# Kernel optimization log

Measured on AMD Instinct MI355X. Metric: run time of the kernel, lower is better.

Reference implementation:

```python
import jax, jax.numpy as jnp
import numpy as np

# Config (matches init_kwargs)
D_MODEL = 1024
D_MLP = 4096
N_EXPERTS = 8
TOP_K = 2  # experts_per_token
BATCH = 1
POS = 2048


def setup_inputs() -> dict:
    key = jax.random.key(0)
    k0, k1, k2, k3, k4 = jax.random.split(key, 5)
    s = 0.02  # typical init scale
    x = jax.random.normal(k0, (BATCH, POS, D_MODEL), jnp.float32)
    W_gate = jax.random.normal(k1, (D_MODEL, N_EXPERTS), jnp.float32) * s  # router
    We_gate = jax.random.normal(k2, (N_EXPERTS, D_MODEL, D_MLP), jnp.float32) * s
    We_in = jax.random.normal(k3, (N_EXPERTS, D_MODEL, D_MLP), jnp.float32) * s
    We_out = jax.random.normal(k4, (N_EXPERTS, D_MLP, D_MODEL), jnp.float32) * s
    return {"x": x, "W_gate": W_gate, "We_gate": We_gate, "We_in": We_in, "We_out": We_out}


def reference(x, W_gate, We_gate, We_in, We_out):
    B, P, D = x.shape
    T = B * P
    E = W_gate.shape[1]
    h = x.reshape(T, D)  # [T, D]

    # Router: logits -> fp32 softmax -> top-k -> renormalize (as in torch code)
    logits = h @ W_gate  # [T, E]
    probs = jax.nn.softmax(logits.astype(jnp.float32), axis=-1)
    topw, topi = jax.lax.top_k(probs, TOP_K)  # [T, K]
    topw = topw / jnp.sum(topw, axis=-1, keepdims=True)
    topw = topw.astype(x.dtype)

    # Per-token combine weight for each expert (0 if not routed). [T, E]
    w_full = jnp.zeros((T, E), x.dtype).at[jnp.arange(T)[:, None], topi].add(topw)

    # Gated-MLP per expert; scan over the small fixed expert axis to avoid
    # materializing [E, T, D_MLP] hidden states at once.
    def per_expert(acc, params):
        Wg, Wi, Wo, we = params  # Wg/Wi: [D, D_MLP], Wo: [D_MLP, D], we: [T]
        hid = jax.nn.silu(h @ Wg) * (h @ Wi)  # [T, D_MLP]
        return acc + (hid @ Wo) * we[:, None], None

    res, _ = jax.lax.scan(
        per_expert,
        jnp.zeros((T, D), x.dtype),
        (We_gate, We_in, We_out, w_full.T),
    )
    return res.reshape(B, P, D)
```

## Files before the change

kernel.cpp:

```cpp
#include <hip/hip_runtime.h>
#include <hip/hip_bf16.h>

#define T_TOK 2048
#define DMODEL 1024
#define DMLP 4096
#define NEXP 8

typedef __bf16 bf16x8 __attribute__((ext_vector_type(8)));
typedef float f32x4 __attribute__((ext_vector_type(4)));
typedef unsigned short u16x8 __attribute__((ext_vector_type(8)));

__device__ __forceinline__ unsigned short f2bf(float f) {
  return __builtin_bit_cast(unsigned short, (__bf16)f);
}

__device__ __forceinline__ void gload16(const unsigned short* g,
                                        unsigned short* l) {
  __builtin_amdgcn_global_load_lds(
      (const __attribute__((address_space(1))) unsigned int*)g,
      (__attribute__((address_space(3))) unsigned int*)l, 16, 0, 0);
}

__global__ __launch_bounds__(64) void router_k(
    const float* __restrict__ x, const float* __restrict__ wg,
    int* __restrict__ topi, float* __restrict__ topw,
    unsigned short* __restrict__ xb) {
  int t = blockIdx.x;
  int lane = threadIdx.x;
  const float* hx = x + (size_t)t * DMODEL;
  float acc[NEXP];
#pragma unroll
  for (int e = 0; e < NEXP; ++e) acc[e] = 0.f;
  for (int i = lane; i < DMODEL; i += 64) {
    float xi = hx[i];
    if (xb) xb[(size_t)t * DMODEL + i] = f2bf(xi);
    const float* w = wg + (size_t)i * NEXP;
#pragma unroll
    for (int e = 0; e < NEXP; ++e) acc[e] += xi * w[e];
  }
#pragma unroll
  for (int off = 32; off > 0; off >>= 1) {
#pragma unroll
    for (int e = 0; e < NEXP; ++e) acc[e] += __shfl_down(acc[e], off);
  }
  if (lane == 0) {
    float m = acc[0];
#pragma unroll
    for (int e = 1; e < NEXP; ++e) m = fmaxf(m, acc[e]);
    float p[NEXP], s = 0.f;
#pragma unroll
    for (int e = 0; e < NEXP; ++e) { p[e] = expf(acc[e] - m); s += p[e]; }
    float inv = 1.f / s;
#pragma unroll
    for (int e = 0; e < NEXP; ++e) p[e] *= inv;
    int i1 = 0;
#pragma unroll
    for (int e = 1; e < NEXP; ++e) if (p[e] > p[i1]) i1 = e;
    int i2 = (i1 == 0) ? 1 : 0;
#pragma unroll
    for (int e = 0; e < NEXP; ++e) if (e != i1 && p[e] > p[i2]) i2 = e;
    float w1 = p[i1], w2 = p[i2];
    float rs = 1.f / (w1 + w2);
    topi[2 * t] = i1;
    topi[2 * t + 1] = i2;
    topw[2 * t] = w1 * rs;
    topw[2 * t + 1] = w2 * rs;
  }
}

__global__ __launch_bounds__(512) void compact_k(
    const int* __restrict__ topi, const float* __restrict__ topw,
    int* __restrict__ offsets, int* __restrict__ perm,
    float* __restrict__ wrow, int* __restrict__ inv) {
  int tid = threadIdx.x;
  int e = tid >> 6, lane = tid & 63;
  __shared__ unsigned char st[2 * T_TOK];
  __shared__ int scnt[NEXP];
  __shared__ int soff[NEXP + 1];
  for (int i = tid; i < (2 * T_TOK) / 4; i += 512) {
    int4 v = ((const int4*)topi)[i];
    uchar4 u;
    u.x = (unsigned char)v.x; u.y = (unsigned char)v.y;
    u.z = (unsigned char)v.z; u.w = (unsigned char)v.w;
    ((uchar4*)st)[i] = u;
  }
  __syncthreads();
  int c = 0;
  for (int j = lane; j < 2 * T_TOK; j += 64) {
    unsigned long long m = __ballot(st[j] == e);
    c += __popcll(m);
  }
  if (lane == 0) scnt[e] = c;
  __syncthreads();
  if (tid == 0) {
    int s = 0;
    for (int k = 0; k < NEXP; ++k) { soff[k] = s; s += scnt[k]; }
    soff[NEXP] = s;
    for (int k = 0; k <= NEXP; ++k) offsets[k] = soff[k];
  }
  __syncthreads();
  int base = soff[e];
  for (int j = lane; j < 2 * T_TOK; j += 64) {
    bool f = (st[j] == e);
    unsigned long long m = __ballot(f);
    if (f) {
      int p = base + __popcll(m & ((1ULL << lane) - 1ULL));
      perm[p] = j >> 1;
      wrow[p] = topw[j];
      inv[j] = p;
    }
    base += __popcll(m);
  }
}

__global__ __launch_bounds__(256) void tpose3_k(
    const float* __restrict__ weg, const float* __restrict__ wei,
    const float* __restrict__ weo, unsigned short* __restrict__ wgt,
    unsigned short* __restrict__ wit, unsigned short* __restrict__ wot) {
  int mat = blockIdx.z;
  int e = blockIdx.y;
  const float* src;
  unsigned short* dst;
  int SK, SN;
  if (mat == 0) { src = weg; dst = wgt; SK = DMODEL; SN = DMLP; }
  else if (mat == 1) { src = wei; dst = wit; SK = DMODEL; SN = DMLP; }
  else { src = weo; dst = wot; SK = DMLP; SN = DMODEL; }
  src += (size_t)e * DMODEL * DMLP;
  dst += (size_t)e * DMODEL * DMLP;
  int ntx = SN >> 6;
  int tile = blockIdx.x;
  int c0 = (tile & (ntx - 1)) * 64, k0 = (tile / ntx) * 64;

  __shared__ unsigned short tl[64 * 64];
  int tid = threadIdx.x;
  int j = tid & 31, g = tid >> 5;
  int r0 = g * 8;

  const float* sp = src + (size_t)(k0 + r0) * SN + c0 + 2 * j;
  float2 v[8];
#pragma unroll
  for (int ri = 0; ri < 8; ++ri) v[ri] = *(const float2*)(sp + (size_t)ri * SN);
#pragma unroll
  for (int i = 0; i < 2; ++i) {
    int cc = 2 * j + i;
    u16x8 p;
#pragma unroll
    for (int ri = 0; ri < 8; ++ri)
      p[ri] = f2bf(i ? v[ri].y : v[ri].x);
    int sl = (g + cc) & 7;
    *(u16x8*)(&tl[cc * 64 + sl * 8]) = p;
  }
  __syncthreads();
#pragma unroll
  for (int i = 0; i < 2; ++i) {
    int task = tid + i * 256;
    int rr = task >> 3, cc = task & 7;
    int sl = (cc + rr) & 7;
    uint4 w = *(const uint4*)(&tl[rr * 64 + sl * 8]);
    *(uint4*)(dst + (size_t)(c0 + rr) * SK + k0 + cc * 8) = w;
  }
}

__global__ __launch_bounds__(256) void hid2_k(
    const unsigned short* __restrict__ xb, const unsigned short* __restrict__ wgt,
    const unsigned short* __restrict__ wit, const int* __restrict__ offsets,
    const int* __restrict__ perm, const float* __restrict__ wrow,
    unsigned short* __restrict__ hid) {
  int e = blockIdx.z;
  int off = offsets[e], end = offsets[e + 1];
  int cnt = end - off;
  int m0 = blockIdx.y * 128;
  if (m0 >= cnt) return;
  int nb = blockIdx.x * 64;

  __shared__ unsigned short As[128 * 32];
  __shared__ unsigned short Bs[128 * 32];

  int tid = threadIdx.x;
  int lane = tid & 63, wid = tid >> 6;
  int wm = (wid & 1) * 64, wn = (wid >> 1) * 64;
  int lr = lane & 15, q = lane >> 4;

  f32x4 acc[4][4];
  f32x4 z = {0.f, 0.f, 0.f, 0.f};
#pragma unroll
  for (int i = 0; i < 4; ++i)
#pragma unroll
    for (int j = 0; j < 4; ++j) acc[i][j] = z;

  const unsigned short* aptr[2];
  const unsigned short* bptr[2];
#pragma unroll
  for (int it = 0; it < 2; ++it) {
    int task = tid + it * 256;
    int r = task >> 2, sp4 = task & 3;
    int ch = (sp4 - (r >> 1)) & 3;
    int pl = m0 + r;
    int src = perm[off + ((pl < cnt) ? pl : 0)];
    aptr[it] = xb + (size_t)src * DMODEL + ch * 8;
    int arr = (r >> 5) & 1;
    int col = nb + (r & 31) + ((r >> 6) << 5);
    const unsigned short* w = (arr ? wit : wgt) + (size_t)e * DMLP * DMODEL;
    bptr[it] = w + (size_t)col * DMODEL + ch * 8;
  }

  for (int k0 = 0; k0 < DMODEL; k0 += 32) {
#pragma unroll
    for (int it = 0; it < 2; ++it) {
      gload16(aptr[it] + k0, &As[(tid + it * 256) * 8]);
      gload16(bptr[it] + k0, &Bs[(tid + it * 256) * 8]);
    }
    __syncthreads();
    bf16x8 af[4], bfr[4];
#pragma unroll
    for (int i = 0; i < 4; ++i) {
      int R = wm + i * 16 + lr;
      af[i] = *(const bf16x8*)(&As[R * 32 + (((q + (R >> 1)) & 3) * 8)]);
    }
#pragma unroll
    for (int j = 0; j < 4; ++j) {
      int R = wn + j * 16 + lr;
      bfr[j] = *(const bf16x8*)(&Bs[R * 32 + (((q + (R >> 1)) & 3) * 8)]);
    }
#pragma unroll
    for (int i = 0; i < 4; ++i)
#pragma unroll
      for (int j = 0; j < 4; ++j)
        acc[i][j] = __builtin_amdgcn_mfma_f32_16x16x32_bf16(af[i], bfr[j],
                                                            acc[i][j], 0, 0, 0);
    __syncthreads();
  }

  int colbase = nb + (wn ? 32 : 0);
#pragma unroll
  for (int i = 0; i < 4; ++i) {
#pragma unroll
    for (int jp = 0; jp < 2; ++jp) {
#pragma unroll
      for (int r = 0; r < 4; ++r) {
        int row = wm + i * 16 + q * 4 + r;
        int pl = m0 + row;
        if (pl < cnt) {
          int pos = off + pl;
          float g = acc[i][jp][r], vv = acc[i][jp + 2][r];
          float hv = (g / (1.f + expf(-g))) * vv * wrow[pos];
          hid[(size_t)pos * DMLP + colbase + jp * 16 + lr] = f2bf(hv);
        }
      }
    }
  }
}

__global__ __launch_bounds__(256) void out2_k(
    const unsigned short* __restrict__ hid, const unsigned short* __restrict__ wot,
    const int* __restrict__ offsets, float* __restrict__ tmp) {
  int e = blockIdx.z;
  int off = offsets[e], end = offsets[e + 1];
  int cnt = end - off;
  int m0 = blockIdx.y * 128;
  if (m0 >= cnt) return;
  int n0 = blockIdx.x * 64;

  __shared__ unsigned short As[128 * 32];
  __shared__ unsigned short Bs[64 * 32];

  int tid = threadIdx.x;
  int lane = tid & 63, wid = tid >> 6;
  int wm = (wid & 1) * 64, wn = (wid >> 1) * 32;
  int lr = lane & 15, q = lane >> 4;

  f32x4 acc[4][2];
  f32x4 z = {0.f, 0.f, 0.f, 0.f};
#pragma unroll
  for (int i = 0; i < 4; ++i)
#pragma unroll
    for (int j = 0; j < 2; ++j) acc[i][j] = z;

  const unsigned short* aptr[2];
  const unsigned short* bptr;
#pragma unroll
  for (int it = 0; it < 2; ++it) {
    int task = tid + it * 256;
    int r = task >> 2, sp4 = task & 3;
    int ch = (sp4 - (r >> 1)) & 3;
    int pl = m0 + r;
    aptr[it] = hid + (size_t)(off + ((pl < cnt) ? pl : 0)) * DMLP + ch * 8;
  }
  {
    int r = tid >> 2, sp4 = tid & 3;
    int ch = (sp4 - (r >> 1)) & 3;
    bptr = wot + (size_t)e * DMODEL * DMLP + (size_t)(n0 + r) * DMLP + ch * 8;
  }

  for (int k0 = 0; k0 < DMLP; k0 += 32) {
#pragma unroll
    for (int it = 0; it < 2; ++it)
      gload16(aptr[it] + k0, &As[(tid + it * 256) * 8]);
    gload16(bptr + k0, &Bs[tid * 8]);
    __syncthreads();
    bf16x8 af[4], bfr[2];
#pragma unroll
    for (int i = 0; i < 4; ++i) {
      int R = wm + i * 16 + lr;
      af[i] = *(const bf16x8*)(&As[R * 32 + (((q + (R >> 1)) & 3) * 8)]);
    }
#pragma unroll
    for (int j = 0; j < 2; ++j) {
      int R = wn + j * 16 + lr;
      bfr[j] = *(const bf16x8*)(&Bs[R * 32 + (((q + (R >> 1)) & 3) * 8)]);
    }
#pragma unroll
    for (int i = 0; i < 4; ++i)
#pragma unroll
      for (int j = 0; j < 2; ++j)
        acc[i][j] = __builtin_amdgcn_mfma_f32_16x16x32_bf16(af[i], bfr[j],
                                                            acc[i][j], 0, 0, 0);
    __syncthreads();
  }

#pragma unroll
  for (int i = 0; i < 4; ++i)
#pragma unroll
    for (int j = 0; j < 2; ++j)
#pragma unroll
      for (int r = 0; r < 4; ++r) {
        int row = wm + i * 16 + q * 4 + r;
        int pl = m0 + row;
        if (pl < cnt) {
          tmp[(size_t)(off + pl) * DMODEL + n0 + wn + j * 16 + lr] =
              acc[i][j][r];
        }
      }
}

__global__ __launch_bounds__(256) void comb_k(const float* __restrict__ tmp,
                                              const int* __restrict__ inv,
                                              float* __restrict__ out) {
  int t = blockIdx.x, c = threadIdx.x;
  int i0 = inv[2 * t], i1 = inv[2 * t + 1];
  const float4* t4 = (const float4*)tmp;
  float4 a = t4[(size_t)i0 * 256 + c];
  float4 b = t4[(size_t)i1 * 256 + c];
  float4 o;
  o.x = a.x + b.x; o.y = a.y + b.y; o.z = a.z + b.z; o.w = a.w + b.w;
  ((float4*)out)[(size_t)t * 256 + c] = o;
}

#define BPITCH 40

__global__ __launch_bounds__(256) void hid_k(
    const float* __restrict__ x, const float* __restrict__ weg,
    const float* __restrict__ wei, const int* __restrict__ offsets,
    const int* __restrict__ perm, const float* __restrict__ wrow,
    unsigned short* __restrict__ hid) {
  int e = blockIdx.z;
  int off = offsets[e], end = offsets[e + 1];
  int cnt = end - off;
  int m0 = blockIdx.y * 128;
  if (m0 >= cnt) return;
  int nb = blockIdx.x * 64;
  const float* wg = weg + (size_t)e * DMODEL * DMLP;
  const float* wi = wei + (size_t)e * DMODEL * DMLP;

  __shared__ unsigned short As[128 * BPITCH];
  __shared__ unsigned short Bg[64 * BPITCH];
  __shared__ unsigned short Bi[64 * BPITCH];

  int tid = threadIdx.x;
  int lane = tid & 63, wid = tid >> 6;
  int wm = (wid & 1) * 64, wn = (wid >> 1) * 32;
  int lr = lane & 15, q = lane >> 4;

  f32x4 accg[4][2], acci[4][2];
  f32x4 z = {0.f, 0.f, 0.f, 0.f};
#pragma unroll
  for (int i = 0; i < 4; ++i)
#pragma unroll
    for (int j = 0; j < 2; ++j) { accg[i][j] = z; acci[i][j] = z; }

  const float* aptr[4];
  int adst[4];
#pragma unroll
  for (int it = 0; it < 4; ++it) {
    int task = tid + it * 256;
    int r = task >> 3, kc = (task & 7) * 4;
    int pl = m0 + r;
    int src = perm[off + ((pl < cnt) ? pl : 0)];
    aptr[it] = x + (size_t)src * DMODEL + kc;
    adst[it] = r * BPITCH + kc;
  }
  int tn = (tid & 15) * 4, tk = (tid >> 4) * 2;

  for (int k0 = 0; k0 < DMODEL; k0 += 32) {
#pragma unroll
    for (int it = 0; it < 4; ++it) {
      float4 v = *(const float4*)(aptr[it] + k0);
      ushort4 u;
      u.x = f2bf(v.x); u.y = f2bf(v.y); u.z = f2bf(v.z); u.w = f2bf(v.w);
      *(ushort4*)(&As[adst[it]]) = u;
    }
    {
      const float* pg = wg + (size_t)(k0 + tk) * DMLP + nb + tn;
      float4 g0 = *(const float4*)(pg);
      float4 g1 = *(const float4*)(pg + DMLP);
      const float* pi = wi + (size_t)(k0 + tk) * DMLP + nb + tn;
      float4 i0 = *(const float4*)(pi);
      float4 i1 = *(const float4*)(pi + DMLP);
      const float* c0 = (const float*)&g0;
      const float* c1 = (const float*)&g1;
      const float* d0 = (const float*)&i0;
      const float* d1 = (const float*)&i1;
#pragma unroll
      for (int cix = 0; cix < 4; ++cix) {
        ushort2 vg; vg.x = f2bf(c0[cix]); vg.y = f2bf(c1[cix]);
        *(ushort2*)(&Bg[(tn + cix) * BPITCH + tk]) = vg;
        ushort2 vi; vi.x = f2bf(d0[cix]); vi.y = f2bf(d1[cix]);
        *(ushort2*)(&Bi[(tn + cix) * BPITCH + tk]) = vi;
      }
    }
    __syncthreads();
    bf16x8 af[4], bgf[2], bif[2];
#pragma unroll
    for (int i = 0; i < 4; ++i)
      af[i] = *(const bf16x8*)(&As[(wm + i * 16 + lr) * BPITCH + q * 8]);
#pragma unroll
    for (int j = 0; j < 2; ++j) {
      bgf[j] = *(const bf16x8*)(&Bg[(wn + j * 16 + lr) * BPITCH + q * 8]);
      bif[j] = *(const bf16x8*)(&Bi[(wn + j * 16 + lr) * BPITCH + q * 8]);
    }
#pragma unroll
    for (int i = 0; i < 4; ++i)
#pragma unroll
      for (int j = 0; j < 2; ++j) {
        accg[i][j] = __builtin_amdgcn_mfma_f32_16x16x32_bf16(af[i], bgf[j], accg[i][j], 0, 0, 0);
        acci[i][j] = __builtin_amdgcn_mfma_f32_16x16x32_bf16(af[i], bif[j], acci[i][j], 0, 0, 0);
      }
    __syncthreads();
  }
#pragma unroll
  for (int i = 0; i < 4; ++i)
#pragma unroll
    for (int j = 0; j < 2; ++j)
#pragma unroll
      for (int r = 0; r < 4; ++r) {
        int row = wm + i * 16 + q * 4 + r;
        int pl = m0 + row;
        if (pl < cnt) {
          int pos = off + pl;
          float g = accg[i][j][r], vv = acci[i][j][r];
          float hv = (g / (1.f + expf(-g))) * vv * wrow[pos];
          hid[(size_t)pos * DMLP + nb + wn + j * 16 + lr] = f2bf(hv);
        }
      }
}

__global__ __launch_bounds__(256) void out_k(
    const unsigned short* __restrict__ hid, const float* __restrict__ weo,
    const int* __restrict__ offsets, const int* __restrict__ perm,
    float* __restrict__ out) {
  int e = blockIdx.z;
  int off = offsets[e], end = offsets[e + 1];
  int cnt = end - off;
  int m0 = blockIdx.y * 128;
  if (m0 >= cnt) return;
  int nb = blockIdx.x * 64;
  const float* wo = weo + (size_t)e * DMLP * DMODEL;

  __shared__ unsigned short As[128 * BPITCH];
  __shared__ unsigned short Bs[64 * BPITCH];

  int tid = threadIdx.x;
  int lane = tid & 63, wid = tid >> 6;
  int wm = (wid & 1) * 64, wn = (wid >> 1) * 32;
  int lr = lane & 15, q = lane >> 4;

  f32x4 acc[4][2];
  f32x4 z = {0.f, 0.f, 0.f, 0.f};
#pragma unroll
  for (int i = 0; i < 4; ++i)
#pragma unroll
    for (int j = 0; j < 2; ++j) acc[i][j] = z;

  const unsigned short* aptr[2];
  int adst[2];
#pragma unroll
  for (int it = 0; it < 2; ++it) {
    int task = tid + it * 256;
    int r = task >> 2, kg = (task & 3) * 8;
    int pl = m0 + r;
    int src = off + ((pl < cnt) ? pl : 0);
    aptr[it] = hid + (size_t)src * DMLP + kg;
    adst[it] = r * BPITCH + kg;
  }
  int tn = (tid & 15) * 4, tk = (tid >> 4) * 2;

  for (int k0 = 0; k0 < DMLP; k0 += 32) {
#pragma unroll
    for (int it = 0; it < 2; ++it) {
      uint4 v = *(const uint4*)(aptr[it] + k0);
      *(uint4*)(&As[adst[it]]) = v;
    }
    {
      const float* pb = wo + (size_t)(k0 + tk) * DMODEL + nb + tn;
      float4 b0 = *(const float4*)(pb);
      float4 b1 = *(const float4*)(pb + DMODEL);
      const float* c0 = (const float*)&b0;
      const float* c1 = (const float*)&b1;
#pragma unroll
      for (int cix = 0; cix < 4; ++cix) {
        ushort2 vb; vb.x = f2bf(c0[cix]); vb.y = f2bf(c1[cix]);
        *(ushort2*)(&Bs[(tn + cix) * BPITCH + tk]) = vb;
      }
    }
    __syncthreads();
    bf16x8 af[4], bf[2];
#pragma unroll
    for (int i = 0; i < 4; ++i)
      af[i] = *(const bf16x8*)(&As[(wm + i * 16 + lr) * BPITCH + q * 8]);
#pragma unroll
    for (int j = 0; j < 2; ++j)
      bf[j] = *(const bf16x8*)(&Bs[(wn + j * 16 + lr) * BPITCH + q * 8]);
#pragma unroll
    for (int i = 0; i < 4; ++i)
#pragma unroll
      for (int j = 0; j < 2; ++j)
        acc[i][j] = __builtin_amdgcn_mfma_f32_16x16x32_bf16(af[i], bf[j], acc[i][j], 0, 0, 0);
    __syncthreads();
  }
#pragma unroll
  for (int i = 0; i < 4; ++i)
#pragma unroll
    for (int j = 0; j < 2; ++j)
#pragma unroll
      for (int r = 0; r < 4; ++r) {
        int row = wm + i * 16 + q * 4 + r;
        int pl = m0 + row;
        if (pl < cnt) {
          int tok = perm[off + pl];
          atomicAdd(&out[(size_t)tok * DMODEL + nb + wn + j * 16 + lr],
                    acc[i][j][r]);
        }
      }
}

extern "C" void kernel_launch(void* const* d_in, const int* in_sizes, int n_in,
                              void* d_out, int out_size, void* d_ws,
                              size_t ws_size, hipStream_t stream) {
  const float* x = (const float*)d_in[0];
  const float* wgate = (const float*)d_in[1];
  const float* weg = (const float*)d_in[2];
  const float* wei = (const float*)d_in[3];
  const float* weo = (const float*)d_in[4];
  float* out = (float*)d_out;

  char* ws = (char*)d_ws;
  const size_t KB = 1024, MB = 1048576;
  int* topi = (int*)(ws + 0 * KB);
  float* topw = (float*)(ws + 16 * KB);
  int* offsets = (int*)(ws + 32 * KB);
  int* perm = (int*)(ws + 33 * KB);
  float* wrow = (float*)(ws + 49 * KB);
  int* inv = (int*)(ws + 65 * KB);

  bool big = ws_size >= (size_t)245 * MB;
  unsigned short* xb = big ? (unsigned short*)(ws + 1 * MB) : nullptr;

  router_k<<<dim3(T_TOK), dim3(64), 0, stream>>>(x, wgate, topi, topw, xb);
  compact_k<<<dim3(1), dim3(512), 0, stream>>>(topi, topw, offsets, perm, wrow, inv);

  if (big) {
    unsigned short* hid = (unsigned short*)(ws + 5 * MB);
    float* tmp = (float*)(ws + 37 * MB);
    unsigned short* wgt = (unsigned short*)(ws + 53 * MB);
    unsigned short* wit = (unsigned short*)(ws + 117 * MB);
    unsigned short* wot = (unsigned short*)(ws + 181 * MB);

    tpose3_k<<<dim3(1024, NEXP, 3), dim3(256), 0, stream>>>(weg, wei, weo,
                                                            wgt, wit, wot);
    hid2_k<<<dim3(DMLP / 64, T_TOK / 128, NEXP), dim3(256), 0, stream>>>(
        xb, wgt, wit, offsets, perm, wrow, hid);
    out2_k<<<dim3(DMODEL / 64, T_TOK / 128, NEXP), dim3(256), 0, stream>>>(
        hid, wot, offsets, tmp);
    comb_k<<<dim3(T_TOK), dim3(256), 0, stream>>>(tmp, inv, out);
  } else {
    unsigned short* hid = (unsigned short*)(ws + 96 * KB);
    hipMemsetAsync(d_out, 0, (size_t)out_size * sizeof(float), stream);
    hid_k<<<dim3(DMLP / 64, T_TOK / 128, NEXP), dim3(256), 0, stream>>>(
        x, weg, wei, offsets, perm, wrow, hid);
    out_k<<<dim3(DMODEL / 64, T_TOK / 128, NEXP), dim3(256), 0, stream>>>(
        hid, weo, offsets, perm, out);
  }
}
```

Baseline: 661.4 us.

## Fuse router with weight transpose, enlarge transpose tiles, deepen GEMM K-step

The router and bf16 cast of x are merged into the weight-transpose launch as an extra grid slice, which saves one kernel launch and lets the router run alongside the transpose. Transpose tiles grow from 64x64 to 128x128. Both grouped GEMMs now stage a 64-wide K slice per barrier instead of 32, halving the number of syncs per tile, and declare a minimum of 4 blocks per CU through launch bounds. This doubles LDS use per block and may raise register pressure.

```diff
diff --git a/kernel.cpp b/kernel.cpp
--- a/kernel.cpp
+++ b/kernel.cpp
@@ -21,50 +21,113 @@
       (__attribute__((address_space(3))) unsigned int*)l, 16, 0, 0);
 }
 
-__global__ __launch_bounds__(64) void router_k(
+__global__ __launch_bounds__(256) void fusedA_k(
     const float* __restrict__ x, const float* __restrict__ wg,
-    int* __restrict__ topi, float* __restrict__ topw,
-    unsigned short* __restrict__ xb) {
-  int t = blockIdx.x;
-  int lane = threadIdx.x;
-  const float* hx = x + (size_t)t * DMODEL;
-  float acc[NEXP];
-#pragma unroll
-  for (int e = 0; e < NEXP; ++e) acc[e] = 0.f;
-  for (int i = lane; i < DMODEL; i += 64) {
-    float xi = hx[i];
-    if (xb) xb[(size_t)t * DMODEL + i] = f2bf(xi);
-    const float* w = wg + (size_t)i * NEXP;
-#pragma unroll
-    for (int e = 0; e < NEXP; ++e) acc[e] += xi * w[e];
-  }
-#pragma unroll
-  for (int off = 32; off > 0; off >>= 1) {
-#pragma unroll
-    for (int e = 0; e < NEXP; ++e) acc[e] += __shfl_down(acc[e], off);
-  }
-  if (lane == 0) {
-    float m = acc[0];
-#pragma unroll
-    for (int e = 1; e < NEXP; ++e) m = fmaxf(m, acc[e]);
-    float p[NEXP], s = 0.f;
-#pragma unroll
-    for (int e = 0; e < NEXP; ++e) { p[e] = expf(acc[e] - m); s += p[e]; }
-    float inv = 1.f / s;
-#pragma unroll
-    for (int e = 0; e < NEXP; ++e) p[e] *= inv;
-    int i1 = 0;
-#pragma unroll
-    for (int e = 1; e < NEXP; ++e) if (p[e] > p[i1]) i1 = e;
-    int i2 = (i1 == 0) ? 1 : 0;
-#pragma unroll
-    for (int e = 0; e < NEXP; ++e) if (e != i1 && p[e] > p[i2]) i2 = e;
-    float w1 = p[i1], w2 = p[i2];
-    float rs = 1.f / (w1 + w2);
-    topi[2 * t] = i1;
-    topi[2 * t + 1] = i2;
-    topw[2 * t] = w1 * rs;
-    topw[2 * t + 1] = w2 * rs;
+    const float* __restrict__ weg, const float* __restrict__ wei,
+    const float* __restrict__ weo, int* __restrict__ topi,
+    float* __restrict__ topw, unsigned short* __restrict__ xb,
+    unsigned short* __restrict__ wgt, unsigned short* __restrict__ wit,
+    unsigned short* __restrict__ wot) {
+  __shared__ unsigned short tl[128 * 128];
+  int tid = threadIdx.x;
+
+  if (blockIdx.z == 3) {
+    int t = blockIdx.y * 256 + blockIdx.x;
+    int lane = tid & 63, wid = tid >> 6;
+    const float* hx = x + (size_t)t * DMODEL;
+    int i0 = tid * 4;
+    float4 v = *(const float4*)(hx + i0);
+    ushort4 u;
+    u.x = f2bf(v.x); u.y = f2bf(v.y); u.z = f2bf(v.z); u.w = f2bf(v.w);
+    *(ushort4*)(xb + (size_t)t * DMODEL + i0) = u;
+    float acc[NEXP];
+#pragma unroll
+    for (int e = 0; e < NEXP; ++e) {
+      acc[e] = v.x * wg[(i0 + 0) * NEXP + e] + v.y * wg[(i0 + 1) * NEXP + e] +
+               v.z * wg[(i0 + 2) * NEXP + e] + v.w * wg[(i0 + 3) * NEXP + e];
+    }
+#pragma unroll
+    for (int off = 32; off > 0; off >>= 1)
+#pragma unroll
+      for (int e = 0; e < NEXP; ++e) acc[e] += __shfl_down(acc[e], off);
+    float* sacc = (float*)tl;
+    if (lane == 0)
+#pragma unroll
+      for (int e = 0; e < NEXP; ++e) sacc[wid * NEXP + e] = acc[e];
+    __syncthreads();
+    if (tid == 0) {
+      float p[NEXP];
+#pragma unroll
+      for (int e = 0; e < NEXP; ++e)
+        p[e] = sacc[e] + sacc[NEXP + e] + sacc[2 * NEXP + e] +
+               sacc[3 * NEXP + e];
+      float m = p[0];
+#pragma unroll
+      for (int e = 1; e < NEXP; ++e) m = fmaxf(m, p[e]);
+      float s = 0.f;
+#pragma unroll
+      for (int e = 0; e < NEXP; ++e) { p[e] = expf(p[e] - m); s += p[e]; }
+      float inv = 1.f / s;
+#pragma unroll
+      for (int e = 0; e < NEXP; ++e) p[e] *= inv;
+      int i1 = 0;
+#pragma unroll
+      for (int e = 1; e < NEXP; ++e) if (p[e] > p[i1]) i1 = e;
+      int i2 = (i1 == 0) ? 1 : 0;
+#pragma unroll
+      for (int e = 0; e < NEXP; ++e) if (e != i1 && p[e] > p[i2]) i2 = e;
+      float w1 = p[i1], w2 = p[i2];
+      float rs = 1.f / (w1 + w2);
+      topi[2 * t] = i1;
+      topi[2 * t + 1] = i2;
+      topw[2 * t] = w1 * rs;
+      topw[2 * t + 1] = w2 * rs;
+    }
+    return;
+  }
+
+  int mat = blockIdx.z, e = blockIdx.y;
+  const float* src;
+  unsigned short* dst;
+  int SK, SN;
+  if (mat == 0) { src = weg; dst = wgt; SK = DMODEL; SN = DMLP; }
+  else if (mat == 1) { src = wei; dst = wit; SK = DMODEL; SN = DMLP; }
+  else { src = weo; dst = wot; SK = DMLP; SN = DMODEL; }
+  src += (size_t)e * DMODEL * DMLP;
+  dst += (size_t)e * DMODEL * DMLP;
+  int ntx = SN >> 7;
+  int tile = blockIdx.x;
+  int c0 = (tile & (ntx - 1)) * 128;
+  int k0 = (tile / ntx) * 128;
+  int j = tid & 63, g = tid >> 6;
+
+#pragma unroll
+  for (int p = 0; p < 4; ++p) {
+    int s = g + p * 4;
+    int r0 = s * 8;
+    const float* sp = src + (size_t)(k0 + r0) * SN + c0 + 2 * j;
+    float2 v[8];
+#pragma unroll
+    for (int ri = 0; ri < 8; ++ri)
+      v[ri] = *(const float2*)(sp + (size_t)ri * SN);
+#pragma unroll
+    for (int i = 0; i < 2; ++i) {
+      int c = 2 * j + i;
+      u16x8 pk;
+#pragma unroll
+      for (int ri = 0; ri < 8; ++ri) pk[ri] = f2bf(i ? v[ri].y : v[ri].x);
+      int sl = (s + c) & 15;
+      *(u16x8*)(&tl[c * 128 + sl * 8]) = pk;
+    }
+  }
+  __syncthreads();
+#pragma unroll
+  for (int p = 0; p < 8; ++p) {
+    int task = tid + p * 256;
+    int rr = task >> 4, cc = task & 15;
+    int sl = (cc + rr) & 15;
+    uint4 w = *(const uint4*)(&tl[rr * 128 + sl * 8]);
+    *(uint4*)(dst + (size_t)(c0 + rr) * SK + k0 + cc * 8) = w;
   }
 }
 
@@ -86,8 +149,8 @@
   }
   __syncthreads();
   int c = 0;
-  for (int j = lane; j < 2 * T_TOK; j += 64) {
-    unsigned long long m = __ballot(st[j] == e);
+  for (int jj = lane; jj < 2 * T_TOK; jj += 64) {
+    unsigned long long m = __ballot(st[jj] == e);
     c += __popcll(m);
   }
   if (lane == 0) scnt[e] = c;
@@ -100,68 +163,20 @@
   }
   __syncthreads();
   int base = soff[e];
-  for (int j = lane; j < 2 * T_TOK; j += 64) {
-    bool f = (st[j] == e);
+  for (int jj = lane; jj < 2 * T_TOK; jj += 64) {
+    bool f = (st[jj] == e);
     unsigned long long m = __ballot(f);
     if (f) {
       int p = base + __popcll(m & ((1ULL << lane) - 1ULL));
-      perm[p] = j >> 1;
-      wrow[p] = topw[j];
-      inv[j] = p;
+      perm[p] = jj >> 1;
+      wrow[p] = topw[jj];
+      inv[jj] = p;
     }
     base += __popcll(m);
   }
 }
 
-__global__ __launch_bounds__(256) void tpose3_k(
-    const float* __restrict__ weg, const float* __restrict__ wei,
-    const float* __restrict__ weo, unsigned short* __restrict__ wgt,
-    unsigned short* __restrict__ wit, unsigned short* __restrict__ wot) {
-  int mat = blockIdx.z;
-  int e = blockIdx.y;
-  const float* src;
-  unsigned short* dst;
-  int SK, SN;
-  if (mat == 0) { src = weg; dst = wgt; SK = DMODEL; SN = DMLP; }
-  else if (mat == 1) { src = wei; dst = wit; SK = DMODEL; SN = DMLP; }
-  else { src = weo; dst = wot; SK = DMLP; SN = DMODEL; }
-  src += (size_t)e * DMODEL * DMLP;
-  dst += (size_t)e * DMODEL * DMLP;
-  int ntx = SN >> 6;
-  int tile = blockIdx.x;
-  int c0 = (tile & (ntx - 1)) * 64, k0 = (tile / ntx) * 64;
-
-  __shared__ unsigned short tl[64 * 64];
-  int tid = threadIdx.x;
-  int j = tid & 31, g = tid >> 5;
-  int r0 = g * 8;
-
-  const float* sp = src + (size_t)(k0 + r0) * SN + c0 + 2 * j;
-  float2 v[8];
-#pragma unroll
-  for (int ri = 0; ri < 8; ++ri) v[ri] = *(const float2*)(sp + (size_t)ri * SN);
-#pragma unroll
-  for (int i = 0; i < 2; ++i) {
-    int cc = 2 * j + i;
-    u16x8 p;
-#pragma unroll
-    for (int ri = 0; ri < 8; ++ri)
-      p[ri] = f2bf(i ? v[ri].y : v[ri].x);
-    int sl = (g + cc) & 7;
-    *(u16x8*)(&tl[cc * 64 + sl * 8]) = p;
-  }
-  __syncthreads();
-#pragma unroll
-  for (int i = 0; i < 2; ++i) {
-    int task = tid + i * 256;
-    int rr = task >> 3, cc = task & 7;
-    int sl = (cc + rr) & 7;
-    uint4 w = *(const uint4*)(&tl[rr * 64 + sl * 8]);
-    *(uint4*)(dst + (size_t)(c0 + rr) * SK + k0 + cc * 8) = w;
-  }
-}
-
-__global__ __launch_bounds__(256) void hid2_k(
+__global__ __launch_bounds__(256, 4) void hid2_k(
     const unsigned short* __restrict__ xb, const unsigned short* __restrict__ wgt,
     const unsigned short* __restrict__ wit, const int* __restrict__ offsets,
     const int* __restrict__ perm, const float* __restrict__ wrow,
@@ -173,8 +188,8 @@
   if (m0 >= cnt) return;
   int nb = blockIdx.x * 64;
 
-  __shared__ unsigned short As[128 * 32];
-  __shared__ unsigned short Bs[128 * 32];
+  __shared__ unsigned short As[128 * 64];
+  __shared__ unsigned short Bs[128 * 64];
 
   int tid = threadIdx.x;
   int lane = tid & 63, wid = tid >> 6;
@@ -186,48 +201,53 @@
 #pragma unroll
   for (int i = 0; i < 4; ++i)
 #pragma unroll
-    for (int j = 0; j < 4; ++j) acc[i][j] = z;
-
-  const unsigned short* aptr[2];
-  const unsigned short* bptr[2];
-#pragma unroll
-  for (int it = 0; it < 2; ++it) {
+    for (int jj = 0; jj < 4; ++jj) acc[i][jj] = z;
+
+  const unsigned short* aptr[4];
+  const unsigned short* bptr[4];
+#pragma unroll
+  for (int it = 0; it < 4; ++it) {
     int task = tid + it * 256;
-    int r = task >> 2, sp4 = task & 3;
-    int ch = (sp4 - (r >> 1)) & 3;
+    int r = task >> 3, sp8 = task & 7;
+    int ch = (sp8 - (r >> 1)) & 7;
     int pl = m0 + r;
-    int src = perm[off + ((pl < cnt) ? pl : 0)];
-    aptr[it] = xb + (size_t)src * DMODEL + ch * 8;
+    int srct = perm[off + ((pl < cnt) ? pl : 0)];
+    aptr[it] = xb + (size_t)srct * DMODEL + ch * 8;
     int arr = (r >> 5) & 1;
     int col = nb + (r & 31) + ((r >> 6) << 5);
     const unsigned short* w = (arr ? wit : wgt) + (size_t)e * DMLP * DMODEL;
     bptr[it] = w + (size_t)col * DMODEL + ch * 8;
   }
 
-  for (int k0 = 0; k0 < DMODEL; k0 += 32) {
-#pragma unroll
-    for (int it = 0; it < 2; ++it) {
+  for (int k0 = 0; k0 < DMODEL; k0 += 64) {
+#pragma unroll
+    for (int it = 0; it < 4; ++it) {
       gload16(aptr[it] + k0, &As[(tid + it * 256) * 8]);
       gload16(bptr[it] + k0, &Bs[(tid + it * 256) * 8]);
     }
     __syncthreads();
-    bf16x8 af[4], bfr[4];
-#pragma unroll
-    for (int i = 0; i < 4; ++i) {
-      int R = wm + i * 16 + lr;
-      af[i] = *(const bf16x8*)(&As[R * 32 + (((q + (R >> 1)) & 3) * 8)]);
-    }
-#pragma unroll
-    for (int j = 0; j < 4; ++j) {
-      int R = wn + j * 16 + lr;
-      bfr[j] = *(const bf16x8*)(&Bs[R * 32 + (((q + (R >> 1)) & 3) * 8)]);
-    }
-#pragma unroll
-    for (int i = 0; i < 4; ++i)
-#pragma unroll
-      for (int j = 0; j < 4; ++j)
-        acc[i][j] = __builtin_amdgcn_mfma_f32_16x16x32_bf16(af[i], bfr[j],
-                                                            acc[i][j], 0, 0, 0);
+#pragma unroll
+    for (int h = 0; h < 2; ++h) {
+      bf16x8 af[4], bfr[4];
+#pragma unroll
+      for (int i = 0; i < 4; ++i) {
+        int R = wm + i * 16 + lr;
+        int sl = ((h * 4 + q) + (R >> 1)) & 7;
+        af[i] = *(const bf16x8*)(&As[R * 64 + sl * 8]);
+      }
+#pragma unroll
+      for (int jj = 0; jj < 4; ++jj) {
+        int R = wn + jj * 16 + lr;
+        int sl = ((h * 4 + q) + (R >> 1)) & 7;
+        bfr[jj] = *(const bf16x8*)(&Bs[R * 64 + sl * 8]);
+      }
+#pragma unroll
+      for (int i = 0; i < 4; ++i)
+#pragma unroll
+        for (int jj = 0; jj < 4; ++jj)
+          acc[i][jj] = __builtin_amdgcn_mfma_f32_16x16x32_bf16(
+              af[i], bfr[jj], acc[i][jj], 0, 0, 0);
+    }
     __syncthreads();
   }
 
@@ -251,7 +271,7 @@
   }
 }
 
-__global__ __launch_bounds__(256) void out2_k(
+__global__ __launch_bounds__(256, 4) void out2_k(
     const unsigned short* __restrict__ hid, const unsigned short* __restrict__ wot,
     const int* __restrict__ offsets, float* __restrict__ tmp) {
   int e = blockIdx.z;
@@ -261,8 +281,8 @@
   if (m0 >= cnt) return;
   int n0 = blockIdx.x * 64;
 
-  __shared__ unsigned short As[128 * 32];
-  __shared__ unsigned short Bs[64 * 32];
+  __shared__ unsigned short As[128 * 64];
+  __shared__ unsigned short Bs[64 * 64];
 
   int tid = threadIdx.x;
   int lane = tid & 63, wid = tid >> 6;
@@ -274,61 +294,70 @@
 #pragma unroll
   for (int i = 0; i < 4; ++i)
 #pragma unroll
-    for (int j = 0; j < 2; ++j) acc[i][j] = z;
-
-  const unsigned short* aptr[2];
-  const unsigned short* bptr;
+    for (int jj = 0; jj < 2; ++jj) acc[i][jj] = z;
+
+  const unsigned short* aptr[4];
+  const unsigned short* bptr[2];
+#pragma unroll
+  for (int it = 0; it < 4; ++it) {
+    int task = tid + it * 256;
+    int r = task >> 3, sp8 = task & 7;
+    int ch = (sp8 - (r >> 1)) & 7;
+    int pl = m0 + r;
+    aptr[it] = hid + (size_t)(off + ((pl < cnt) ? pl : 0)) * DMLP + ch * 8;
+  }
 #pragma unroll
   for (int it = 0; it < 2; ++it) {
     int task = tid + it * 256;
-    int r = task >> 2, sp4 = task & 3;
-    int ch = (sp4 - (r >> 1)) & 3;
-    int pl = m0 + r;
-    aptr[it] = hid + (size_t)(off + ((pl < cnt) ? pl : 0)) * DMLP + ch * 8;
-  }
-  {
-    int r = tid >> 2, sp4 = tid & 3;
-    int ch = (sp4 - (r >> 1)) & 3;
-    bptr = wot + (size_t)e * DMODEL * DMLP + (size_t)(n0 + r) * DMLP + ch * 8;
-  }
-
-  for (int k0 = 0; k0 < DMLP; k0 += 32) {
+    int r = task >> 3, sp8 = task & 7;
+    int ch = (sp8 - (r >> 1)) & 7;
+    bptr[it] = wot + (size_t)e * DMODEL * DMLP + (size_t)(n0 + r) * DMLP + ch * 8;
+  }
+
+  for (int k0 = 0; k0 < DMLP; k0 += 64) {
+#pragma unroll
+    for (int it = 0; it < 4; ++it)
+      gload16(aptr[it] + k0, &As[(tid + it * 256) * 8]);
 #pragma unroll
     for (int it = 0; it < 2; ++it)
-      gload16(aptr[it] + k0, &As[(tid + it * 256) * 8]);
-    gload16(bptr + k0, &Bs[tid * 8]);
-    __syncthreads();
-    bf16x8 af[4], bfr[2];
-#pragma unroll
-    for (int i = 0; i < 4; ++i) {
-      int R = wm + i * 16 + lr;
-      af[i] = *(const bf16x8*)(&As[R * 32 + (((q + (R >> 1)) & 3) * 8)]);
-    }
-#pragma unroll
-    for (int j = 0; j < 2; ++j) {
-      int R = wn + j * 16 + lr;
-      bfr[j] = *(const bf16x8*)(&Bs[R * 32 + (((q + (R >> 1)) & 3) * 8)]);
-    }
-#pragma unroll
-    for (int i = 0; i < 4; ++i)
-#pragma unroll
-      for (int j = 0; j < 2; ++j)
-        acc[i][j] = __builtin_amdgcn_mfma_f32_16x16x32_bf16(af[i], bfr[j],
-                                                            acc[i][j], 0, 0, 0);
+      gload16(bptr[it] + k0, &Bs[(tid + it * 256) * 8]);
+    __syncthreads();
+#pragma unroll
+    for (int h = 0; h < 2; ++h) {
+      bf16x8 af[4], bfr[2];
+#pragma unroll
+      for (int i = 0; i < 4; ++i) {
+        int R = wm + i * 16 + lr;
+        int sl = ((h * 4 + q) + (R >> 1)) & 7;
+        af[i] = *(const bf16x8*)(&As[R * 64 + sl * 8]);
+      }
+#pragma unroll
+      for (int jj = 0; jj < 2; ++jj) {
+        int R = wn + jj * 16 + lr;
+        int sl = ((h * 4 + q) + (R >> 1)) & 7;
+        bfr[jj] = *(const bf16x8*)(&Bs[R * 64 + sl * 8]);
+      }
+#pragma unroll
+      for (int i = 0; i < 4; ++i)
+#pragma unroll
+        for (int jj = 0; jj < 2; ++jj)
+          acc[i][jj] = __builtin_amdgcn_mfma_f32_16x16x32_bf16(
+              af[i], bfr[jj], acc[i][jj], 0, 0, 0);
+    }
     __syncthreads();
   }
 
 #pragma unroll
   for (int i = 0; i < 4; ++i)
 #pragma unroll
-    for (int j = 0; j < 2; ++j)
+    for (int jj = 0; jj < 2; ++jj)
 #pragma unroll
       for (int r = 0; r < 4; ++r) {
         int row = wm + i * 16 + q * 4 + r;
         int pl = m0 + row;
         if (pl < cnt) {
-          tmp[(size_t)(off + pl) * DMODEL + n0 + wn + j * 16 + lr] =
-              acc[i][j][r];
+          tmp[(size_t)(off + pl) * DMODEL + n0 + wn + jj * 16 + lr] =
+              acc[i][jj][r];
         }
       }
 }
@@ -347,6 +376,51 @@
 }
 
 #define BPITCH 40
+
+__global__ __launch_bounds__(64) void router_k(
+    const float* __restrict__ x, const float* __restrict__ wg,
+    int* __restrict__ topi, float* __restrict__ topw) {
+  int t = blockIdx.x;
+  int lane = threadIdx.x;
+  const float* hx = x + (size_t)t * DMODEL;
+  float acc[NEXP];
+#pragma unroll
+  for (int e = 0; e < NEXP; ++e) acc[e] = 0.f;
+  for (int i = lane; i < DMODEL; i += 64) {
+    float xi = hx[i];
+    const float* w = wg + (size_t)i * NEXP;
+#pragma unroll
+    for (int e = 0; e < NEXP; ++e) acc[e] += xi * w[e];
+  }
+#pragma unroll
+  for (int off = 32; off > 0; off >>= 1) {
+#pragma unroll
+    for (int e = 0; e < NEXP; ++e) acc[e] += __shfl_down(acc[e], off);
+  }
+  if (lane == 0) {
+    float m = acc[0];
+#pragma unroll
+    for (int e = 1; e < NEXP; ++e) m = fmaxf(m, acc[e]);
+    float p[NEXP], s = 0.f;
+#pragma unroll
+    for (int e = 0; e < NEXP; ++e) { p[e] = expf(acc[e] - m); s += p[e]; }
+    float inv = 1.f / s;
+#pragma unroll
+    for (int e = 0; e < NEXP; ++e) p[e] *= inv;
+    int i1 = 0;
+#pragma unroll
+    for (int e = 1; e < NEXP; ++e) if (p[e] > p[i1]) i1 = e;
+    int i2 = (i1 == 0) ? 1 : 0;
+#pragma unroll
+    for (int e = 0; e < NEXP; ++e) if (e != i1 && p[e] > p[i2]) i2 = e;
+    float w1 = p[i1], w2 = p[i2];
+    float rs = 1.f / (w1 + w2);
+    topi[2 * t] = i1;
+    topi[2 * t + 1] = i2;
+    topw[2 * t] = w1 * rs;
+    topw[2 * t + 1] = w2 * rs;
+  }
+}
 
 __global__ __launch_bounds__(256) void hid_k(
     const float* __restrict__ x, const float* __restrict__ weg,
@@ -563,20 +637,19 @@
   int* inv = (int*)(ws + 65 * KB);
 
   bool big = ws_size >= (size_t)245 * MB;
-  unsigned short* xb = big ? (unsigned short*)(ws + 1 * MB) : nullptr;
-
-  router_k<<<dim3(T_TOK), dim3(64), 0, stream>>>(x, wgate, topi, topw, xb);
-  compact_k<<<dim3(1), dim3(512), 0, stream>>>(topi, topw, offsets, perm, wrow, inv);
 
   if (big) {
+    unsigned short* xb = (unsigned short*)(ws + 1 * MB);
     unsigned short* hid = (unsigned short*)(ws + 5 * MB);
     float* tmp = (float*)(ws + 37 * MB);
     unsigned short* wgt = (unsigned short*)(ws + 53 * MB);
     unsigned short* wit = (unsigned short*)(ws + 117 * MB);
     unsigned short* wot = (unsigned short*)(ws + 181 * MB);
 
-    tpose3_k<<<dim3(1024, NEXP, 3), dim3(256), 0, stream>>>(weg, wei, weo,
-                                                            wgt, wit, wot);
+    fusedA_k<<<dim3(256, NEXP, 4), dim3(256), 0, stream>>>(
+        x, wgate, weg, wei, weo, topi, topw, xb, wgt, wit, wot);
+    compact_k<<<dim3(1), dim3(512), 0, stream>>>(topi, topw, offsets, perm,
+                                                 wrow, inv);
     hid2_k<<<dim3(DMLP / 64, T_TOK / 128, NEXP), dim3(256), 0, stream>>>(
         xb, wgt, wit, offsets, perm, wrow, hid);
     out2_k<<<dim3(DMODEL / 64, T_TOK / 128, NEXP), dim3(256), 0, stream>>>(
@@ -585,6 +658,9 @@
   } else {
     unsigned short* hid = (unsigned short*)(ws + 96 * KB);
     hipMemsetAsync(d_out, 0, (size_t)out_size * sizeof(float), stream);
+    router_k<<<dim3(T_TOK), dim3(64), 0, stream>>>(x, wgate, topi, topw);
+    compact_k<<<dim3(1), dim3(512), 0, stream>>>(topi, topw, offsets, perm,
+                                                 wrow, inv);
     hid_k<<<dim3(DMLP / 64, T_TOK / 128, NEXP), dim3(256), 0, stream>>>(
         x, weg, wei, offsets, perm, wrow, hid);
     out_k<<<dim3(DMODEL / 64, T_TOK / 128, NEXP), dim3(256), 0, stream>>>(
```

New measurement: 713.7 us. 1.08x slower.
